# Optimization experiments

Hardware: AMD Instinct MI355X
Metric: run time of the kernel (lower is better)

Reference implementation:

```python
import jax, jax.numpy as jnp
import numpy as np

N_SRC0, N_DST0, N_DST1 = 100000, 50000, 25000
E0, E1, D = 1600000, 800000, 128


def setup_inputs() -> dict:
    key = jax.random.key(0)
    k = jax.random.split(key, 8)
    return {
        "x": jax.random.normal(k[0], (N_SRC0, D), dtype=jnp.float32),
        "src0": jax.random.randint(k[1], (E0,), 0, N_SRC0, dtype=jnp.int32),
        "dst0": jax.random.randint(k[2], (E0,), 0, N_DST0, dtype=jnp.int32),
        "ew0": jax.random.uniform(k[3], (E0,), dtype=jnp.float32),
        "src1": jax.random.randint(k[4], (E1,), 0, N_DST0, dtype=jnp.int32),
        "dst1": jax.random.randint(k[5], (E1,), 0, N_DST1, dtype=jnp.int32),
        "ew1": jax.random.uniform(k[6], (E1,), dtype=jnp.float32),
        "n_dst0": N_DST0,
        "n_dst1": N_DST1,
    }


def _propagate(h, src, dst, ew, n_dst):
    # u_mul_e: gather src feature per edge and scale by edge weight; sum-reduce to dst
    m = h[src] * ew[:, None]                      # [E, D]
    return jax.ops.segment_sum(m, dst, num_segments=n_dst)  # [n_dst, D]


def reference(x, src0, dst0, ew0, src1, dst1, ew1, n_dst0, n_dst1):
    # LightGCN forward over 2 sampled blocks, mlp_list=None
    h = _propagate(x, src0, dst0, ew0, n_dst0)    # [n_dst0, D]
    h = _propagate(h, src1, dst1, ew1, n_dst1)    # [n_dst1, D]
    return h
```

## Files before the change

kernel.cpp:

```cpp
#include <hip/hip_runtime.h>


#define DIMS 128
#define BK   64
#define BKSH 6
#define CAP  4096
#define CH   8192

__device__ __forceinline__ unsigned bf16_1(float a) {
  unsigned u = __float_as_uint(a);
  return (u + 0x7fffu + ((u >> 16) & 1u)) >> 16;
}
__device__ __forceinline__ unsigned pack_bf16(float a, float b) {
  return bf16_1(a) | (bf16_1(b) << 16);
}

__global__ __launch_bounds__(256) void hist_cvt(
    const int* __restrict__ dst0, const int* __restrict__ dst1,
    const float* __restrict__ xf, uint4* __restrict__ xbf4,
    int* __restrict__ wgcnt0, int* __restrict__ wgcnt1,
    int E0, int E1, int NB0, int NB1, int NW0, int NW1, long long n8) {
  int b = blockIdx.x;
  if (b < NW0 + NW1) {
    __shared__ int hist[1024];
    const int s1 = (b >= NW0);
    const int w  = s1 ? b - NW0 : b;
    const int E  = s1 ? E1 : E0;
    const int NB = s1 ? NB1 : NB0;
    const int* dst = s1 ? dst1 : dst0;
    int* wgcnt = s1 ? wgcnt1 : wgcnt0;
    for (int i = threadIdx.x; i < NB; i += 256) hist[i] = 0;
    __syncthreads();
    const int beg = w * CH, end = min(beg + CH, E);
    for (int e = beg + threadIdx.x; e < end; e += 256)
      atomicAdd(&hist[dst[e] >> BKSH], 1);
    __syncthreads();
    for (int i = threadIdx.x; i < NB; i += 256)
      wgcnt[w * NB + i] = hist[i];
  } else {
    long long t = (long long)(b - NW0 - NW1) * 256 + threadIdx.x;
    if (t < n8) {
      const float4* xf4 = (const float4*)xf;
      float4 v0 = xf4[t * 2], v1 = xf4[t * 2 + 1];
      xbf4[t] = make_uint4(pack_bf16(v0.x, v0.y), pack_bf16(v0.z, v0.w),
                           pack_bf16(v1.x, v1.y), pack_bf16(v1.z, v1.w));
    }
  }
}

__global__ __launch_bounds__(256) void scan_cols(
    int* __restrict__ wgcnt0, int* __restrict__ wgcnt1,
    int* __restrict__ tot0, int* __restrict__ tot1,
    int NB0, int NB1, int NW0, int NW1) {
  __shared__ int part[256];
  int b = blockIdx.x;
  const int s1 = (b >= NB0);
  const int i = s1 ? b - NB0 : b;
  int* wgcnt = s1 ? wgcnt1 : wgcnt0;
  int* tot   = s1 ? tot1 : tot0;
  const int NB = s1 ? NB1 : NB0;
  const int NW = s1 ? NW1 : NW0;
  const int t = threadIdx.x;
  int v = (t < NW) ? wgcnt[t * NB + i] : 0;
  part[t] = v;
  __syncthreads();
  for (int off = 1; off < 256; off <<= 1) {
    int u = (t >= off) ? part[t - off] : 0;
    __syncthreads();
    part[t] += u;
    __syncthreads();
  }
  if (t < NW) wgcnt[t * NB + i] = part[t] - v;
  if (t == 255) tot[i] = part[255];
}

__global__ __launch_bounds__(1024) void scan_tot(
    const int* __restrict__ tot0, const int* __restrict__ tot1,
    int2* __restrict__ rg0, int2* __restrict__ rg1, int NB0, int NB1) {
  __shared__ int part[1024];
  const int s1 = blockIdx.x;
  const int* tot = s1 ? tot1 : tot0;
  int2* rg = s1 ? rg1 : rg0;
  const int NB = s1 ? NB1 : NB0;
  const int t = threadIdx.x;
  int v = (t < NB) ? tot[t] : 0;
  part[t] = v;
  __syncthreads();
  for (int off = 1; off < 1024; off <<= 1) {
    int u = (t >= off) ? part[t - off] : 0;
    __syncthreads();
    part[t] += u;
    __syncthreads();
  }
  if (t < NB) rg[t] = make_int2(part[t] - v, part[t]);
}

__global__ __launch_bounds__(512) void partition_k(
    const int* __restrict__ src0, const int* __restrict__ dst0,
    const float* __restrict__ ew0, const int* __restrict__ src1,
    const int* __restrict__ dst1, const float* __restrict__ ew1,
    const int* __restrict__ wgcnt0, const int* __restrict__ wgcnt1,
    const int2* __restrict__ rg0, const int2* __restrict__ rg1,
    int2* __restrict__ payl0, int2* __restrict__ payl1,
    int E0, int E1, int NB0, int NB1, int NW0, int NW1) {
  __shared__ int cur[1024];
  int b = blockIdx.x;
  const int s1 = (b >= NW0);
  const int w  = s1 ? b - NW0 : b;
  const int E  = s1 ? E1 : E0;
  const int NB = s1 ? NB1 : NB0;
  const int* src = s1 ? src1 : src0;
  const int* dst = s1 ? dst1 : dst0;
  const float* ew = s1 ? ew1 : ew0;
  const int* wgcnt = s1 ? wgcnt1 : wgcnt0;
  const int2* rg = s1 ? rg1 : rg0;
  int2* payl = s1 ? payl1 : payl0;
  for (int i = threadIdx.x; i < NB; i += 512)
    cur[i] = rg[i].x + wgcnt[w * NB + i];
  __syncthreads();
  const int beg = w * CH, end = min(beg + CH, E);
  for (int e = beg + threadIdx.x; e < end; e += 512) {
    int d = dst[e];
    int pos = atomicAdd(&cur[d >> BKSH], 1);
    payl[pos] = make_int2(src[e],
                          (int)((bf16_1(ew[e]) << 16) | (unsigned)(d & (BK - 1))));
  }
}

template <bool OUT_BF16>
__global__ __launch_bounds__(512) void gather_bkt(
    const uint4* __restrict__ feat, const int2* __restrict__ rg,
    const int2* __restrict__ payl, void* __restrict__ outp, int n_dst) {
  __shared__ int2 lp[CAP];
  __shared__ int cnt[BK], base[BK], cnt2[BK];
  const int b = blockIdx.x;
  const int tid = threadIdx.x;
  const int2 r = rg[b];
  const int n = r.y - r.x;
  const int nin = min(n, CAP);
  if (tid < BK) { cnt[tid] = 0; cnt2[tid] = 0; }
  __syncthreads();
  for (int j = tid; j < nin; j += 512)
    atomicAdd(&cnt[payl[r.x + j].y & (BK - 1)], 1);
  __syncthreads();
  if (tid < 64) {
    int v = cnt[tid];
    int s = v;
    for (int off = 1; off < 64; off <<= 1) {
      int u = __shfl_up(s, off);
      if (tid >= off) s += u;
    }
    base[tid] = s - v;
  }
  __syncthreads();
  for (int j = tid; j < nin; j += 512) {
    int2 p = payl[r.x + j];
    int dl = p.y & (BK - 1);
    int pos = base[dl] + atomicAdd(&cnt2[dl], 1);
    lp[pos] = p;
  }
  __syncthreads();
  const int wave = tid >> 6;
  const int lane = tid & 63;
  const int rr = lane >> 4;
  const int c  = lane & 15;
  for (int dl = wave; dl < BK; dl += 8) {
    const int row = b * BK + dl;
    if (row >= n_dst) break;
    const int bg = base[dl];
    const int en = bg + cnt[dl];
    float a0 = 0.f, a1 = 0.f, a2 = 0.f, a3 = 0.f;
    float a4 = 0.f, a5 = 0.f, a6 = 0.f, a7 = 0.f;
    for (int j = bg; j < en; j += 4) {
      int jj = j + rr;
      int2 p = (jj < en) ? lp[jj] : make_int2(0, 0);
      float wgt = __uint_as_float((unsigned)p.y & 0xffff0000u);
      uint4 u = feat[(size_t)p.x * 16 + c];
      a0 += __uint_as_float(u.x << 16) * wgt;
      a1 += __uint_as_float(u.x & 0xffff0000u) * wgt;
      a2 += __uint_as_float(u.y << 16) * wgt;
      a3 += __uint_as_float(u.y & 0xffff0000u) * wgt;
      a4 += __uint_as_float(u.z << 16) * wgt;
      a5 += __uint_as_float(u.z & 0xffff0000u) * wgt;
      a6 += __uint_as_float(u.w << 16) * wgt;
      a7 += __uint_as_float(u.w & 0xffff0000u) * wgt;
    }
    if (n > CAP) {
      for (int j = CAP; j < n; j += 4) {
        int jj = j + rr;
        int2 p = (jj < n) ? payl[r.x + jj] : make_int2(0, 0);
        bool mine = (jj < n) && ((p.y & (BK - 1)) == dl);
        float wgt = mine ? __uint_as_float((unsigned)p.y & 0xffff0000u) : 0.f;
        uint4 u = feat[(size_t)p.x * 16 + c];
        a0 += __uint_as_float(u.x << 16) * wgt;
        a1 += __uint_as_float(u.x & 0xffff0000u) * wgt;
        a2 += __uint_as_float(u.y << 16) * wgt;
        a3 += __uint_as_float(u.y & 0xffff0000u) * wgt;
        a4 += __uint_as_float(u.z << 16) * wgt;
        a5 += __uint_as_float(u.z & 0xffff0000u) * wgt;
        a6 += __uint_as_float(u.w << 16) * wgt;
        a7 += __uint_as_float(u.w & 0xffff0000u) * wgt;
      }
    }
    a0 += __shfl_xor(a0, 16); a0 += __shfl_xor(a0, 32);
    a1 += __shfl_xor(a1, 16); a1 += __shfl_xor(a1, 32);
    a2 += __shfl_xor(a2, 16); a2 += __shfl_xor(a2, 32);
    a3 += __shfl_xor(a3, 16); a3 += __shfl_xor(a3, 32);
    a4 += __shfl_xor(a4, 16); a4 += __shfl_xor(a4, 32);
    a5 += __shfl_xor(a5, 16); a5 += __shfl_xor(a5, 32);
    a6 += __shfl_xor(a6, 16); a6 += __shfl_xor(a6, 32);
    a7 += __shfl_xor(a7, 16); a7 += __shfl_xor(a7, 32);
    if (OUT_BF16) {
      if (rr == 0) {
        ((uint4*)outp)[(size_t)row * 16 + c] =
            make_uint4(pack_bf16(a0, a1), pack_bf16(a2, a3),
                       pack_bf16(a4, a5), pack_bf16(a6, a7));
      }
    } else {
      if (rr < 2) {
        ((float4*)outp)[(size_t)row * 32 + c * 2 + rr] =
            (rr == 0) ? make_float4(a0, a1, a2, a3)
                      : make_float4(a4, a5, a6, a7);
      }
    }
  }
}

#define COLG 32
__global__ __launch_bounds__(256) void prop_atomic(
    const float* __restrict__ x, const int* __restrict__ src,
    const int* __restrict__ dst, const float* __restrict__ ew,
    float* __restrict__ out, int E) {
  long long idx = (long long)blockIdx.x * blockDim.x + threadIdx.x;
  long long total = (long long)E * COLG;
  if (idx >= total) return;
  int e = (int)(idx >> 5);
  int cg = (int)(idx & 31);
  int s = src[e];
  int d = dst[e];
  float w = ew[e];
  const float4 v = *reinterpret_cast<const float4*>(x + (size_t)s * DIMS + cg * 4);
  float* o = out + (size_t)d * DIMS + cg * 4;
  atomicAdd(o + 0, v.x * w);
  atomicAdd(o + 1, v.y * w);
  atomicAdd(o + 2, v.z * w);
  atomicAdd(o + 3, v.w * w);
}


static inline size_t align_up(size_t v, size_t a) { return (v + a - 1) / a * a; }

extern "C" void kernel_launch(void* const* d_in, const int* in_sizes, int n_in,
                              void* d_out, int out_size, void* d_ws, size_t ws_size,
                              hipStream_t stream) {
  const float* x    = (const float*)d_in[0];
  const int*   src0 = (const int*)d_in[1];
  const int*   dst0 = (const int*)d_in[2];
  const float* ew0  = (const float*)d_in[3];
  const int*   src1 = (const int*)d_in[4];
  const int*   dst1 = (const int*)d_in[5];
  const float* ew1  = (const float*)d_in[6];

  const int N_SRC0 = in_sizes[0] / DIMS;
  const int E0 = in_sizes[1];
  const int E1 = in_sizes[4];
  const int N_DST0 = 50000;
  const int N_DST1 = 25000;

  const int NB0 = (N_DST0 + BK - 1) / BK;
  const int NB1 = (N_DST1 + BK - 1) / BK;
  const int NW0 = (E0 + CH - 1) / CH;
  const int NW1 = (E1 + CH - 1) / CH;

  float* out = (float*)d_out;

  char* ws = (char*)d_ws;
  size_t off = 0;
  uint4* xb    = (uint4*)(ws + off); off = align_up(off + (size_t)N_SRC0 * 64 * 4, 16);
  uint4* hb    = (uint4*)(ws + off); off = align_up(off + (size_t)N_DST0 * 64 * 4, 16);
  int* wgcnt0  = (int*)(ws + off);   off = align_up(off + (size_t)NW0 * NB0 * 4, 16);
  int* wgcnt1  = (int*)(ws + off);   off = align_up(off + (size_t)NW1 * NB1 * 4, 16);
  int* tot0    = (int*)(ws + off);   off = align_up(off + (size_t)NB0 * 4, 16);
  int* tot1    = (int*)(ws + off);   off = align_up(off + (size_t)NB1 * 4, 16);
  int2* rg0    = (int2*)(ws + off);  off = align_up(off + (size_t)NB0 * 8, 16);
  int2* rg1    = (int2*)(ws + off);  off = align_up(off + (size_t)NB1 * 8, 16);
  int2* payl0  = (int2*)(ws + off);  off = align_up(off + (size_t)E0 * 8, 16);
  int2* payl1  = (int2*)(ws + off);  off = align_up(off + (size_t)E1 * 8, 16);
  const size_t needed = off;

  if (ws_size < needed) {
    float* h = (float*)d_ws;
    hipMemsetAsync(h, 0, (size_t)N_DST0 * DIMS * 4, stream);
    hipMemsetAsync(out, 0, (size_t)N_DST1 * DIMS * 4, stream);
    long long t0 = (long long)E0 * COLG;
    prop_atomic<<<(int)((t0 + 255) / 256), 256, 0, stream>>>(x, src0, dst0, ew0, h, E0);
    long long t1 = (long long)E1 * COLG;
    prop_atomic<<<(int)((t1 + 255) / 256), 256, 0, stream>>>(h, src1, dst1, ew1, out, E1);
    return;
  }

  const long long n8 = (long long)N_SRC0 * 16;
  const int cvtBlocks = (int)((n8 + 255) / 256);

  hist_cvt<<<NW0 + NW1 + cvtBlocks, 256, 0, stream>>>(
      dst0, dst1, x, xb, wgcnt0, wgcnt1, E0, E1, NB0, NB1, NW0, NW1, n8);

  scan_cols<<<NB0 + NB1, 256, 0, stream>>>(wgcnt0, wgcnt1, tot0, tot1,
                                           NB0, NB1, NW0, NW1);

  scan_tot<<<2, 1024, 0, stream>>>(tot0, tot1, rg0, rg1, NB0, NB1);

  partition_k<<<NW0 + NW1, 512, 0, stream>>>(
      src0, dst0, ew0, src1, dst1, ew1, wgcnt0, wgcnt1, rg0, rg1,
      payl0, payl1, E0, E1, NB0, NB1, NW0, NW1);

  gather_bkt<true><<<NB0, 512, 0, stream>>>(xb, rg0, payl0, (void*)hb, N_DST0);

  gather_bkt<false><<<NB1, 512, 0, stream>>>(hb, rg1, payl1, (void*)out, N_DST1);
}
```

Before: 159.0 us.

## Split gather buckets across two blocks and replace total scan with atomic offsets

The scan_tot kernel is removed. Each bucket's base offset in the payload is now claimed with a global atomicAdd in scan_cols, which saves one launch but makes bucket order non-deterministic. The gather kernel runs two blocks per 64-row bucket, each handling 32 destination rows. This doubles the block count and shrinks the shared staging buffer, but each block still reads the whole bucket payload to filter its half. The inner accumulate loop is also unrolled by two, so two feature loads are in flight per iteration.

```diff
diff --git a/kernel.cpp b/kernel.cpp
--- a/kernel.cpp
+++ b/kernel.cpp
@@ -4,7 +4,7 @@
 #define DIMS 128
 #define BK   64
 #define BKSH 6
-#define CAP  4096
+#define CAP2 2048
 #define CH   8192
 
 __device__ __forceinline__ unsigned bf16_1(float a) {
@@ -50,14 +50,14 @@
 
 __global__ __launch_bounds__(256) void scan_cols(
     int* __restrict__ wgcnt0, int* __restrict__ wgcnt1,
-    int* __restrict__ tot0, int* __restrict__ tot1,
+    int* __restrict__ gcur, int2* __restrict__ rg0, int2* __restrict__ rg1,
     int NB0, int NB1, int NW0, int NW1) {
   __shared__ int part[256];
   int b = blockIdx.x;
   const int s1 = (b >= NB0);
   const int i = s1 ? b - NB0 : b;
   int* wgcnt = s1 ? wgcnt1 : wgcnt0;
-  int* tot   = s1 ? tot1 : tot0;
+  int2* rg   = s1 ? rg1 : rg0;
   const int NB = s1 ? NB1 : NB0;
   const int NW = s1 ? NW1 : NW0;
   const int t = threadIdx.x;
@@ -71,28 +71,11 @@
     __syncthreads();
   }
   if (t < NW) wgcnt[t * NB + i] = part[t] - v;
-  if (t == 255) tot[i] = part[255];
-}
-
-__global__ __launch_bounds__(1024) void scan_tot(
-    const int* __restrict__ tot0, const int* __restrict__ tot1,
-    int2* __restrict__ rg0, int2* __restrict__ rg1, int NB0, int NB1) {
-  __shared__ int part[1024];
-  const int s1 = blockIdx.x;
-  const int* tot = s1 ? tot1 : tot0;
-  int2* rg = s1 ? rg1 : rg0;
-  const int NB = s1 ? NB1 : NB0;
-  const int t = threadIdx.x;
-  int v = (t < NB) ? tot[t] : 0;
-  part[t] = v;
-  __syncthreads();
-  for (int off = 1; off < 1024; off <<= 1) {
-    int u = (t >= off) ? part[t - off] : 0;
-    __syncthreads();
-    part[t] += u;
-    __syncthreads();
-  }
-  if (t < NB) rg[t] = make_int2(part[t] - v, part[t]);
+  if (t == 255) {
+    int tot = part[255];
+    int base = atomicAdd(&gcur[s1], tot);
+    rg[i] = make_int2(base, base + tot);
+  }
 }
 
 __global__ __launch_bounds__(512) void partition_k(
@@ -128,68 +111,91 @@
 }
 
 template <bool OUT_BF16>
-__global__ __launch_bounds__(512) void gather_bkt(
+__global__ __launch_bounds__(512) void gather_half(
     const uint4* __restrict__ feat, const int2* __restrict__ rg,
     const int2* __restrict__ payl, void* __restrict__ outp, int n_dst) {
-  __shared__ int2 lp[CAP];
-  __shared__ int cnt[BK], base[BK], cnt2[BK];
-  const int b = blockIdx.x;
-  const int tid = threadIdx.x;
+  __shared__ int2 lp[CAP2];
+  __shared__ int cnt[32], base[32], cnt2[32];
+  __shared__ int nf_sh;
+  const int b    = blockIdx.x >> 1;
+  const int half = blockIdx.x & 1;
+  const int tid  = threadIdx.x;
   const int2 r = rg[b];
   const int n = r.y - r.x;
-  const int nin = min(n, CAP);
-  if (tid < BK) { cnt[tid] = 0; cnt2[tid] = 0; }
-  __syncthreads();
-  for (int j = tid; j < nin; j += 512)
-    atomicAdd(&cnt[payl[r.x + j].y & (BK - 1)], 1);
-  __syncthreads();
-  if (tid < 64) {
+  if (tid < 32) { cnt[tid] = 0; cnt2[tid] = 0; }
+  __syncthreads();
+  for (int j = tid; j < n; j += 512) {
+    int dl = payl[r.x + j].y & (BK - 1);
+    if ((dl >> 5) == half) atomicAdd(&cnt[dl & 31], 1);
+  }
+  __syncthreads();
+  if (tid < 32) {
     int v = cnt[tid];
     int s = v;
-    for (int off = 1; off < 64; off <<= 1) {
+    for (int off = 1; off < 32; off <<= 1) {
       int u = __shfl_up(s, off);
       if (tid >= off) s += u;
     }
     base[tid] = s - v;
-  }
-  __syncthreads();
-  for (int j = tid; j < nin; j += 512) {
-    int2 p = payl[r.x + j];
-    int dl = p.y & (BK - 1);
-    int pos = base[dl] + atomicAdd(&cnt2[dl], 1);
-    lp[pos] = p;
+    if (tid == 31) nf_sh = s;
+  }
+  __syncthreads();
+  const int nf = nf_sh;
+  if (nf <= CAP2) {
+    for (int j = tid; j < n; j += 512) {
+      int2 p = payl[r.x + j];
+      int dl = p.y & (BK - 1);
+      if ((dl >> 5) == half) {
+        int pos = base[dl & 31] + atomicAdd(&cnt2[dl & 31], 1);
+        lp[pos] = p;
+      }
+    }
   }
   __syncthreads();
   const int wave = tid >> 6;
   const int lane = tid & 63;
   const int rr = lane >> 4;
   const int c  = lane & 15;
-  for (int dl = wave; dl < BK; dl += 8) {
-    const int row = b * BK + dl;
+  for (int dl2 = wave; dl2 < 32; dl2 += 8) {
+    const int row = b * BK + half * 32 + dl2;
     if (row >= n_dst) break;
-    const int bg = base[dl];
-    const int en = bg + cnt[dl];
     float a0 = 0.f, a1 = 0.f, a2 = 0.f, a3 = 0.f;
     float a4 = 0.f, a5 = 0.f, a6 = 0.f, a7 = 0.f;
-    for (int j = bg; j < en; j += 4) {
-      int jj = j + rr;
-      int2 p = (jj < en) ? lp[jj] : make_int2(0, 0);
-      float wgt = __uint_as_float((unsigned)p.y & 0xffff0000u);
-      uint4 u = feat[(size_t)p.x * 16 + c];
-      a0 += __uint_as_float(u.x << 16) * wgt;
-      a1 += __uint_as_float(u.x & 0xffff0000u) * wgt;
-      a2 += __uint_as_float(u.y << 16) * wgt;
-      a3 += __uint_as_float(u.y & 0xffff0000u) * wgt;
-      a4 += __uint_as_float(u.z << 16) * wgt;
-      a5 += __uint_as_float(u.z & 0xffff0000u) * wgt;
-      a6 += __uint_as_float(u.w << 16) * wgt;
-      a7 += __uint_as_float(u.w & 0xffff0000u) * wgt;
-    }
-    if (n > CAP) {
-      for (int j = CAP; j < n; j += 4) {
+    if (nf <= CAP2) {
+      const int bg = base[dl2];
+      const int en = bg + cnt[dl2];
+      for (int j = bg; j < en; j += 8) {
+        int jj0 = j + rr;
+        int jj1 = j + 4 + rr;
+        int2 p0 = (jj0 < en) ? lp[jj0] : make_int2(0, 0);
+        int2 p1 = (jj1 < en) ? lp[jj1] : make_int2(0, 0);
+        float w0 = __uint_as_float((unsigned)p0.y & 0xffff0000u);
+        float w1 = __uint_as_float((unsigned)p1.y & 0xffff0000u);
+        uint4 u0 = feat[(size_t)p0.x * 16 + c];
+        uint4 u1 = feat[(size_t)p1.x * 16 + c];
+        a0 += __uint_as_float(u0.x << 16) * w0;
+        a1 += __uint_as_float(u0.x & 0xffff0000u) * w0;
+        a2 += __uint_as_float(u0.y << 16) * w0;
+        a3 += __uint_as_float(u0.y & 0xffff0000u) * w0;
+        a4 += __uint_as_float(u0.z << 16) * w0;
+        a5 += __uint_as_float(u0.z & 0xffff0000u) * w0;
+        a6 += __uint_as_float(u0.w << 16) * w0;
+        a7 += __uint_as_float(u0.w & 0xffff0000u) * w0;
+        a0 += __uint_as_float(u1.x << 16) * w1;
+        a1 += __uint_as_float(u1.x & 0xffff0000u) * w1;
+        a2 += __uint_as_float(u1.y << 16) * w1;
+        a3 += __uint_as_float(u1.y & 0xffff0000u) * w1;
+        a4 += __uint_as_float(u1.z << 16) * w1;
+        a5 += __uint_as_float(u1.z & 0xffff0000u) * w1;
+        a6 += __uint_as_float(u1.w << 16) * w1;
+        a7 += __uint_as_float(u1.w & 0xffff0000u) * w1;
+      }
+    } else {
+      const int want = half * 32 + dl2;
+      for (int j = 0; j < n; j += 4) {
         int jj = j + rr;
         int2 p = (jj < n) ? payl[r.x + jj] : make_int2(0, 0);
-        bool mine = (jj < n) && ((p.y & (BK - 1)) == dl);
+        bool mine = (jj < n) && ((p.y & (BK - 1)) == want);
         float wgt = mine ? __uint_as_float((unsigned)p.y & 0xffff0000u) : 0.f;
         uint4 u = feat[(size_t)p.x * 16 + c];
         a0 += __uint_as_float(u.x << 16) * wgt;
@@ -280,8 +286,7 @@
   uint4* hb    = (uint4*)(ws + off); off = align_up(off + (size_t)N_DST0 * 64 * 4, 16);
   int* wgcnt0  = (int*)(ws + off);   off = align_up(off + (size_t)NW0 * NB0 * 4, 16);
   int* wgcnt1  = (int*)(ws + off);   off = align_up(off + (size_t)NW1 * NB1 * 4, 16);
-  int* tot0    = (int*)(ws + off);   off = align_up(off + (size_t)NB0 * 4, 16);
-  int* tot1    = (int*)(ws + off);   off = align_up(off + (size_t)NB1 * 4, 16);
+  int* gcur    = (int*)(ws + off);   off = align_up(off + 2 * 4, 16);
   int2* rg0    = (int2*)(ws + off);  off = align_up(off + (size_t)NB0 * 8, 16);
   int2* rg1    = (int2*)(ws + off);  off = align_up(off + (size_t)NB1 * 8, 16);
   int2* payl0  = (int2*)(ws + off);  off = align_up(off + (size_t)E0 * 8, 16);
@@ -302,19 +307,19 @@
   const long long n8 = (long long)N_SRC0 * 16;
   const int cvtBlocks = (int)((n8 + 255) / 256);
 
+  hipMemsetAsync(gcur, 0, 2 * 4, stream);
+
   hist_cvt<<<NW0 + NW1 + cvtBlocks, 256, 0, stream>>>(
       dst0, dst1, x, xb, wgcnt0, wgcnt1, E0, E1, NB0, NB1, NW0, NW1, n8);
 
-  scan_cols<<<NB0 + NB1, 256, 0, stream>>>(wgcnt0, wgcnt1, tot0, tot1,
+  scan_cols<<<NB0 + NB1, 256, 0, stream>>>(wgcnt0, wgcnt1, gcur, rg0, rg1,
                                            NB0, NB1, NW0, NW1);
-
-  scan_tot<<<2, 1024, 0, stream>>>(tot0, tot1, rg0, rg1, NB0, NB1);
 
   partition_k<<<NW0 + NW1, 512, 0, stream>>>(
       src0, dst0, ew0, src1, dst1, ew1, wgcnt0, wgcnt1, rg0, rg1,
       payl0, payl1, E0, E1, NB0, NB1, NW0, NW1);
 
-  gather_bkt<true><<<NB0, 512, 0, stream>>>(xb, rg0, payl0, (void*)hb, N_DST0);
-
-  gather_bkt<false><<<NB1, 512, 0, stream>>>(hb, rg1, payl1, (void*)out, N_DST1);
-}
+  gather_half<true><<<2 * NB0, 512, 0, stream>>>(xb, rg0, payl0, (void*)hb, N_DST0);
+
+  gather_half<false><<<2 * NB1, 512, 0, stream>>>(hb, rg1, payl1, (void*)out, N_DST1);
+}
```

New measurement: 165.8 us. 1.04x slower.

## Replace bucket-total scan kernel with atomic offsets and unroll gather loop by four

Applied to the files above, without the earlier changes.

Drops the separate scan_tot kernel. Each bucket's base offset now comes from an atomicAdd on a global cursor inside scan_cols, so buckets are placed in arbitrary order rather than prefix order, and a small memset is added to reset the cursor. Separately, the gather inner loop is unrolled four ways so each lane issues four independent feature loads before accumulating, which should raise memory-level parallelism. The cost is a memset launch, more register pressure in gather_bkt, and non-deterministic bucket layout in the payload array.

```diff
diff --git a/kernel.cpp b/kernel.cpp
--- a/kernel.cpp
+++ b/kernel.cpp
@@ -50,14 +50,14 @@
 
 __global__ __launch_bounds__(256) void scan_cols(
     int* __restrict__ wgcnt0, int* __restrict__ wgcnt1,
-    int* __restrict__ tot0, int* __restrict__ tot1,
+    int* __restrict__ gcur, int2* __restrict__ rg0, int2* __restrict__ rg1,
     int NB0, int NB1, int NW0, int NW1) {
   __shared__ int part[256];
   int b = blockIdx.x;
   const int s1 = (b >= NB0);
   const int i = s1 ? b - NB0 : b;
   int* wgcnt = s1 ? wgcnt1 : wgcnt0;
-  int* tot   = s1 ? tot1 : tot0;
+  int2* rg   = s1 ? rg1 : rg0;
   const int NB = s1 ? NB1 : NB0;
   const int NW = s1 ? NW1 : NW0;
   const int t = threadIdx.x;
@@ -71,28 +71,11 @@
     __syncthreads();
   }
   if (t < NW) wgcnt[t * NB + i] = part[t] - v;
-  if (t == 255) tot[i] = part[255];
-}
-
-__global__ __launch_bounds__(1024) void scan_tot(
-    const int* __restrict__ tot0, const int* __restrict__ tot1,
-    int2* __restrict__ rg0, int2* __restrict__ rg1, int NB0, int NB1) {
-  __shared__ int part[1024];
-  const int s1 = blockIdx.x;
-  const int* tot = s1 ? tot1 : tot0;
-  int2* rg = s1 ? rg1 : rg0;
-  const int NB = s1 ? NB1 : NB0;
-  const int t = threadIdx.x;
-  int v = (t < NB) ? tot[t] : 0;
-  part[t] = v;
-  __syncthreads();
-  for (int off = 1; off < 1024; off <<= 1) {
-    int u = (t >= off) ? part[t - off] : 0;
-    __syncthreads();
-    part[t] += u;
-    __syncthreads();
-  }
-  if (t < NB) rg[t] = make_int2(part[t] - v, part[t]);
+  if (t == 255) {
+    int tot = part[255];
+    int base = atomicAdd(&gcur[s1], tot);
+    rg[i] = make_int2(base, base + tot);
+  }
 }
 
 __global__ __launch_bounds__(512) void partition_k(
@@ -127,6 +110,18 @@
   }
 }
 
+#define EDGE_BLOCK(p, wgt, u)                                   \
+  {                                                             \
+    a0 += __uint_as_float((u).x << 16) * (wgt);                 \
+    a1 += __uint_as_float((u).x & 0xffff0000u) * (wgt);         \
+    a2 += __uint_as_float((u).y << 16) * (wgt);                 \
+    a3 += __uint_as_float((u).y & 0xffff0000u) * (wgt);         \
+    a4 += __uint_as_float((u).z << 16) * (wgt);                 \
+    a5 += __uint_as_float((u).z & 0xffff0000u) * (wgt);         \
+    a6 += __uint_as_float((u).w << 16) * (wgt);                 \
+    a7 += __uint_as_float((u).w & 0xffff0000u) * (wgt);         \
+  }
+
 template <bool OUT_BF16>
 __global__ __launch_bounds__(512) void gather_bkt(
     const uint4* __restrict__ feat, const int2* __restrict__ rg,
@@ -171,19 +166,27 @@
     const int en = bg + cnt[dl];
     float a0 = 0.f, a1 = 0.f, a2 = 0.f, a3 = 0.f;
     float a4 = 0.f, a5 = 0.f, a6 = 0.f, a7 = 0.f;
-    for (int j = bg; j < en; j += 4) {
-      int jj = j + rr;
-      int2 p = (jj < en) ? lp[jj] : make_int2(0, 0);
-      float wgt = __uint_as_float((unsigned)p.y & 0xffff0000u);
-      uint4 u = feat[(size_t)p.x * 16 + c];
-      a0 += __uint_as_float(u.x << 16) * wgt;
-      a1 += __uint_as_float(u.x & 0xffff0000u) * wgt;
-      a2 += __uint_as_float(u.y << 16) * wgt;
-      a3 += __uint_as_float(u.y & 0xffff0000u) * wgt;
-      a4 += __uint_as_float(u.z << 16) * wgt;
-      a5 += __uint_as_float(u.z & 0xffff0000u) * wgt;
-      a6 += __uint_as_float(u.w << 16) * wgt;
-      a7 += __uint_as_float(u.w & 0xffff0000u) * wgt;
+    for (int j = bg; j < en; j += 16) {
+      const int jj0 = j + rr;
+      const int jj1 = j + 4 + rr;
+      const int jj2 = j + 8 + rr;
+      const int jj3 = j + 12 + rr;
+      int2 p0 = (jj0 < en) ? lp[jj0] : make_int2(0, 0);
+      int2 p1 = (jj1 < en) ? lp[jj1] : make_int2(0, 0);
+      int2 p2 = (jj2 < en) ? lp[jj2] : make_int2(0, 0);
+      int2 p3 = (jj3 < en) ? lp[jj3] : make_int2(0, 0);
+      uint4 u0 = feat[(size_t)p0.x * 16 + c];
+      uint4 u1 = feat[(size_t)p1.x * 16 + c];
+      uint4 u2 = feat[(size_t)p2.x * 16 + c];
+      uint4 u3 = feat[(size_t)p3.x * 16 + c];
+      float w0 = __uint_as_float((unsigned)p0.y & 0xffff0000u);
+      float w1 = __uint_as_float((unsigned)p1.y & 0xffff0000u);
+      float w2 = __uint_as_float((unsigned)p2.y & 0xffff0000u);
+      float w3 = __uint_as_float((unsigned)p3.y & 0xffff0000u);
+      EDGE_BLOCK(p0, w0, u0);
+      EDGE_BLOCK(p1, w1, u1);
+      EDGE_BLOCK(p2, w2, u2);
+      EDGE_BLOCK(p3, w3, u3);
     }
     if (n > CAP) {
       for (int j = CAP; j < n; j += 4) {
@@ -192,14 +195,7 @@
         bool mine = (jj < n) && ((p.y & (BK - 1)) == dl);
         float wgt = mine ? __uint_as_float((unsigned)p.y & 0xffff0000u) : 0.f;
         uint4 u = feat[(size_t)p.x * 16 + c];
-        a0 += __uint_as_float(u.x << 16) * wgt;
-        a1 += __uint_as_float(u.x & 0xffff0000u) * wgt;
-        a2 += __uint_as_float(u.y << 16) * wgt;
-        a3 += __uint_as_float(u.y & 0xffff0000u) * wgt;
-        a4 += __uint_as_float(u.z << 16) * wgt;
-        a5 += __uint_as_float(u.z & 0xffff0000u) * wgt;
-        a6 += __uint_as_float(u.w << 16) * wgt;
-        a7 += __uint_as_float(u.w & 0xffff0000u) * wgt;
+        EDGE_BLOCK(p, wgt, u);
       }
     }
     a0 += __shfl_xor(a0, 16); a0 += __shfl_xor(a0, 32);
@@ -280,8 +276,7 @@
   uint4* hb    = (uint4*)(ws + off); off = align_up(off + (size_t)N_DST0 * 64 * 4, 16);
   int* wgcnt0  = (int*)(ws + off);   off = align_up(off + (size_t)NW0 * NB0 * 4, 16);
   int* wgcnt1  = (int*)(ws + off);   off = align_up(off + (size_t)NW1 * NB1 * 4, 16);
-  int* tot0    = (int*)(ws + off);   off = align_up(off + (size_t)NB0 * 4, 16);
-  int* tot1    = (int*)(ws + off);   off = align_up(off + (size_t)NB1 * 4, 16);
+  int* gcur    = (int*)(ws + off);   off = align_up(off + 2 * 4, 16);
   int2* rg0    = (int2*)(ws + off);  off = align_up(off + (size_t)NB0 * 8, 16);
   int2* rg1    = (int2*)(ws + off);  off = align_up(off + (size_t)NB1 * 8, 16);
   int2* payl0  = (int2*)(ws + off);  off = align_up(off + (size_t)E0 * 8, 16);
@@ -302,13 +297,13 @@
   const long long n8 = (long long)N_SRC0 * 16;
   const int cvtBlocks = (int)((n8 + 255) / 256);
 
+  hipMemsetAsync(gcur, 0, 2 * 4, stream);
+
   hist_cvt<<<NW0 + NW1 + cvtBlocks, 256, 0, stream>>>(
       dst0, dst1, x, xb, wgcnt0, wgcnt1, E0, E1, NB0, NB1, NW0, NW1, n8);
 
-  scan_cols<<<NB0 + NB1, 256, 0, stream>>>(wgcnt0, wgcnt1, tot0, tot1,
+  scan_cols<<<NB0 + NB1, 256, 0, stream>>>(wgcnt0, wgcnt1, gcur, rg0, rg1,
                                            NB0, NB1, NW0, NW1);
-
-  scan_tot<<<2, 1024, 0, stream>>>(tot0, tot1, rg0, rg1, NB0, NB1);
 
   partition_k<<<NW0 + NW1, 512, 0, stream>>>(
       src0, dst0, ew0, src1, dst1, ew1, wgcnt0, wgcnt1, rg0, rg1,
```

Result: slower. 168.9 us (+6.2%).
